# Optimization experiments

Hardware: AMD Instinct MI355X
Metric: run time of the kernel (lower is better)

## Reference

```python
import jax, jax.numpy as jnp
import numpy as np

N = 100000          # num nodes
E = 1_600_000       # num edges (avg degree 16)
IN = 512
OUT = 64
HOPS = 4


def setup_inputs() -> dict:
    key = jax.random.key(0)
    k1, k2, k3 = jax.random.split(key, 3)
    x = jax.random.normal(k1, (N, IN), dtype=jnp.float32)
    W = jax.random.normal(k2, (OUT, IN), dtype=jnp.float32) * 0.02
    b = jnp.zeros((OUT,), dtype=jnp.float32)
    edge_index = jax.random.randint(k3, (2, E), 0, N, dtype=jnp.int32)
    return {"x": x, "W": W, "b": b, "edge_index": edge_index}


def reference(x, W, b, edge_index):
    # 1) linear projection first (low-memory SGC variant)
    h = x @ W.T + b                      # [N, OUT]
    n = h.shape[0]

    # 2) gcn_norm: add self loops, symmetric D^{-1/2} A D^{-1/2}
    row, col = edge_index[0], edge_index[1]
    loop = jnp.arange(n, dtype=row.dtype)
    row = jnp.concatenate([row, loop])   # [E+N]
    col = jnp.concatenate([col, loop])
    ew = jnp.ones(row.shape[0], dtype=h.dtype)
    deg = jax.ops.segment_sum(ew, col, num_segments=n)          # in-degree incl. self loop
    dinv = jnp.where(deg > 0, jax.lax.rsqrt(deg), 0.0)
    w = dinv[row] * ew * dinv[col]       # normalized edge weights [E+N]

    # 3) hops x SpMM: adj_t built with (row=col, col=row) => out[col] += w * h[row]
    for _ in range(HOPS):
        h = jax.ops.segment_sum(w[:, None] * h[row], col, num_segments=n)
    return h
```

## Files before the change

kernel.cpp:

```cpp
#include <hip/hip_runtime.h>
#include <stdint.h>

#define IN_DIM 512
#define OUT_DIM 64

typedef short bf16x8 __attribute__((ext_vector_type(8)));
typedef float f32x4 __attribute__((ext_vector_type(4)));

__device__ inline unsigned short f2bf(float f) {
    unsigned int u = __float_as_uint(f);
    return (unsigned short)((u + 0x7FFFu + ((u >> 16) & 1u)) >> 16);
}
__device__ inline float bf2f(unsigned short s) {
    return __uint_as_float(((unsigned int)s) << 16);
}

__global__ void zero_deg_kernel(int* __restrict__ deg, int N) {
    int i = blockIdx.x * blockDim.x + threadIdx.x;
    if (i < N) deg[i] = 0;
}

__global__ void hist_kernel(const int* __restrict__ col, int* __restrict__ deg, int E) {
    int i = blockIdx.x * blockDim.x + threadIdx.x;
    if (i < E) atomicAdd(&deg[col[i]], 1);
}

__global__ void dinv_kernel(const int* __restrict__ deg, float* __restrict__ dinv,
                            float* __restrict__ d2, int N) {
    int i = blockIdx.x * blockDim.x + threadIdx.x;
    if (i < N) {
        float d = (float)deg[i] + 1.0f;
        dinv[i] = 1.0f / sqrtf(d);
        d2[i] = 1.0f / d;
    }
}

__global__ void pack_w_kernel(const float* __restrict__ W,
                              unsigned short* __restrict__ Bhi,
                              unsigned short* __restrict__ Blo) {
    int tid = blockIdx.x * blockDim.x + threadIdx.x;
    if (tid >= 4096) return;
    int L = tid & 63;
    int ct = tid >> 6;
    int t = ct & 15, c = ct >> 4;
    int o = c * 16 + (L & 15);
    int k0 = t * 32 + (L >> 4) * 8;
    const float* src = W + (size_t)o * IN_DIM + k0;
    #pragma unroll
    for (int j = 0; j < 8; ++j) {
        float w = src[j];
        unsigned short h = f2bf(w);
        Bhi[(size_t)tid * 8 + j] = h;
        Blo[(size_t)tid * 8 + j] = f2bf(w - bf2f(h));
    }
}

__global__ __launch_bounds__(1024) void scan_kernel(const int* __restrict__ deg,
                                                    int* __restrict__ rowptr,
                                                    int* __restrict__ cursor, int N) {
    __shared__ int sm[17];
    int tid = threadIdx.x, lane = tid & 63, wid = tid >> 6;
    if (tid == 0) sm[16] = 0;
    __syncthreads();
    for (int base = 0; base < N; base += 4096) {
        int i = base + tid * 4;
        int4 v = make_int4(0, 0, 0, 0);
        if (i + 3 < N) {
            v = *(const int4*)(deg + i);
        } else {
            if (i < N) v.x = deg[i];
            if (i + 1 < N) v.y = deg[i + 1];
            if (i + 2 < N) v.z = deg[i + 2];
            if (i + 3 < N) v.w = deg[i + 3];
        }
        int s1 = v.x, s2 = s1 + v.y, s3 = s2 + v.z, s4 = s3 + v.w;
        int incl = s4;
        #pragma unroll
        for (int d = 1; d < 64; d <<= 1) {
            int t = __shfl_up(incl, d, 64);
            if (lane >= d) incl += t;
        }
        __syncthreads();
        if (lane == 63) sm[wid] = incl;
        __syncthreads();
        if (tid == 0) {
            int run = sm[16];
            #pragma unroll
            for (int w2 = 0; w2 < 16; ++w2) { int t = sm[w2]; sm[w2] = run; run += t; }
            sm[16] = run;
        }
        __syncthreads();
        int tbase = incl - s4 + sm[wid];
        if (i + 3 < N) {
            int4 o = make_int4(tbase, tbase + s1, tbase + s2, tbase + s3);
            *(int4*)(rowptr + i) = o;
            *(int4*)(cursor + i) = o;
        } else {
            if (i < N)     { rowptr[i]     = tbase;      cursor[i]     = tbase; }
            if (i + 1 < N) { rowptr[i + 1] = tbase + s1; cursor[i + 1] = tbase + s1; }
            if (i + 2 < N) { rowptr[i + 2] = tbase + s2; cursor[i + 2] = tbase + s2; }
            if (i + 3 < N) { rowptr[i + 3] = tbase + s3; cursor[i + 3] = tbase + s3; }
        }
    }
    __syncthreads();
    if (tid == 0) rowptr[N] = sm[16];
}

__global__ void fill_kernel(const int* __restrict__ row, const int* __restrict__ col,
                            int* __restrict__ cursor, int* __restrict__ csr, int E) {
    int i = blockIdx.x * blockDim.x + threadIdx.x;
    if (i < E) {
        int r = row[i], c = col[i];
        int pos = atomicAdd(&cursor[c], 1);
        csr[pos] = r;
    }
}

__global__ __launch_bounds__(256) void mfma_gemm_kernel(const float* __restrict__ x,
                                                        const unsigned short* __restrict__ Bhi,
                                                        const unsigned short* __restrict__ Blo,
                                                        const float* __restrict__ bias,
                                                        const float* __restrict__ dinv,
                                                        float* __restrict__ h, int N) {
    int lane = threadIdx.x & 63;
    int wid  = __builtin_amdgcn_readfirstlane(threadIdx.x >> 6);
    int quad = lane >> 4, r16 = lane & 15;
    long rowBase = ((long)blockIdx.x * 4 + wid) * 32;
    if (rowBase >= N) return;
    bool full = (rowBase + 32 <= N);

    f32x4 acc[2][4];
    #pragma unroll
    for (int rt = 0; rt < 2; ++rt)
        #pragma unroll
        for (int c = 0; c < 4; ++c) acc[rt][c] = (f32x4){0.f, 0.f, 0.f, 0.f};

    int row0 = (int)rowBase + r16;
    int row1 = (int)rowBase + 16 + r16;
    int row0c = full ? row0 : (row0 < N ? row0 : N - 1);
    int row1c = full ? row1 : (row1 < N ? row1 : N - 1);
    const float* a0p = x + (size_t)row0c * IN_DIM + quad * 8;
    const float* a1p = x + (size_t)row1c * IN_DIM + quad * 8;

    for (int t = 0; t < 16; ++t) {
        bf16x8 bh[4], bl[4];
        #pragma unroll
        for (int c = 0; c < 4; ++c) {
            size_t off = ((size_t)(c * 16 + t) * 64 + lane) * 8;
            union { int4 i; bf16x8 b; } uh, ul;
            uh.i = *(const int4*)(Bhi + off);
            ul.i = *(const int4*)(Blo + off);
            bh[c] = uh.b; bl[c] = ul.b;
        }
        bf16x8 ah[2], al[2];
        #pragma unroll
        for (int rt = 0; rt < 2; ++rt) {
            const float* p = (rt ? a1p : a0p) + t * 32;
            float4 f0 = *(const float4*)p;
            float4 f1 = *(const float4*)(p + 4);
            float v[8] = {f0.x, f0.y, f0.z, f0.w, f1.x, f1.y, f1.z, f1.w};
            #pragma unroll
            for (int j = 0; j < 8; ++j) {
                unsigned short hi = f2bf(v[j]);
                ah[rt][j] = (short)hi;
                al[rt][j] = (short)f2bf(v[j] - bf2f(hi));
            }
        }
        #pragma unroll
        for (int rt = 0; rt < 2; ++rt)
            #pragma unroll
            for (int c = 0; c < 4; ++c) {
                acc[rt][c] = __builtin_amdgcn_mfma_f32_16x16x32_bf16(ah[rt], bh[c], acc[rt][c], 0, 0, 0);
                acc[rt][c] = __builtin_amdgcn_mfma_f32_16x16x32_bf16(ah[rt], bl[c], acc[rt][c], 0, 0, 0);
                acc[rt][c] = __builtin_amdgcn_mfma_f32_16x16x32_bf16(al[rt], bh[c], acc[rt][c], 0, 0, 0);
            }
    }

    float bb[4];
    #pragma unroll
    for (int c = 0; c < 4; ++c) bb[c] = bias[c * 16 + r16];
    #pragma unroll
    for (int rt = 0; rt < 2; ++rt)
        #pragma unroll
        for (int rr = 0; rr < 4; ++rr) {
            int row = (int)rowBase + rt * 16 + quad * 4 + rr;
            if (row < N) {
                float dv = dinv[row];
                #pragma unroll
                for (int c = 0; c < 4; ++c)
                    h[(size_t)row * OUT_DIM + c * 16 + r16] = dv * (acc[rt][c][rr] + bb[c]);
            }
        }
}

__global__ __launch_bounds__(256) void hop_kernel(const float* __restrict__ src,
                                                  float* __restrict__ dst,
                                                  const int* __restrict__ csr,
                                                  const int* __restrict__ rowptr,
                                                  const float* __restrict__ scale, int N) {
    int lane = threadIdx.x & 63;
    int wid = __builtin_amdgcn_readfirstlane(threadIdx.x >> 6);
    int node = blockIdx.x * 4 + wid;
    if (node >= N) return;
    float acc = src[(size_t)node * OUT_DIM + lane];
    int s = rowptr[node], e = rowptr[node + 1];
    int i = s;
    for (; i + 16 <= e; i += 16) {
        int idx[16];
        #pragma unroll
        for (int j = 0; j < 16; ++j) idx[j] = csr[i + j];
        float v[16];
        #pragma unroll
        for (int j = 0; j < 16; ++j) v[j] = src[(size_t)idx[j] * OUT_DIM + lane];
        float t0 = ((v[0] + v[1]) + (v[2] + v[3])) + ((v[4] + v[5]) + (v[6] + v[7]));
        float t1 = ((v[8] + v[9]) + (v[10] + v[11])) + ((v[12] + v[13]) + (v[14] + v[15]));
        acc += t0 + t1;
    }
    for (; i + 4 <= e; i += 4) {
        int i0 = csr[i], i1 = csr[i + 1], i2 = csr[i + 2], i3 = csr[i + 3];
        float v0 = src[(size_t)i0 * OUT_DIM + lane];
        float v1 = src[(size_t)i1 * OUT_DIM + lane];
        float v2 = src[(size_t)i2 * OUT_DIM + lane];
        float v3 = src[(size_t)i3 * OUT_DIM + lane];
        acc += (v0 + v1) + (v2 + v3);
    }
    for (; i < e; ++i) acc += src[(size_t)csr[i] * OUT_DIM + lane];
    dst[(size_t)node * OUT_DIM + lane] = scale[node] * acc;
}

extern "C" void kernel_launch(void* const* d_in, const int* in_sizes, int n_in,
                              void* d_out, int out_size, void* d_ws, size_t ws_size,
                              hipStream_t stream) {
    const float* x  = (const float*)d_in[0];
    const float* W  = (const float*)d_in[1];
    const float* b  = (const float*)d_in[2];
    const int*   ei = (const int*)d_in[3];
    int N = in_sizes[0] / IN_DIM;
    int E = in_sizes[3] / 2;
    const int* row = ei;
    const int* col = ei + E;
    float* out = (float*)d_out;

    float* dinv   = (float*)d_ws;
    float* d2     = dinv + N;
    int*   deg    = (int*)(d2 + N);
    int*   rowptr = deg + N;
    int*   cursor = rowptr + (N + 4);
    unsigned short* Bhi = (unsigned short*)(cursor + N);
    unsigned short* Blo = Bhi + 32768;

    float* xspace = (float*)d_in[0];
    float* hbuf   = xspace;
    int*   csr    = (int*)(xspace + (size_t)N * OUT_DIM);

    dim3 blk(256);
    int gN = (N + 255) / 256;
    int gE = (E + 255) / 256;

    zero_deg_kernel<<<gN, blk, 0, stream>>>(deg, N);
    hist_kernel<<<gE, blk, 0, stream>>>(col, deg, E);
    dinv_kernel<<<gN, blk, 0, stream>>>(deg, dinv, d2, N);

    pack_w_kernel<<<16, blk, 0, stream>>>(W, Bhi, Blo);

    mfma_gemm_kernel<<<(N + 127) / 128, blk, 0, stream>>>(x, Bhi, Blo, b, dinv, out, N);

    scan_kernel<<<1, 1024, 0, stream>>>(deg, rowptr, cursor, N);
    fill_kernel<<<gE, blk, 0, stream>>>(row, col, cursor, csr, E);

    int gH = (N + 3) / 4;
    hop_kernel<<<gH, blk, 0, stream>>>(out, hbuf, csr, rowptr, d2, N);
    hop_kernel<<<gH, blk, 0, stream>>>(hbuf, out, csr, rowptr, d2, N);
    hop_kernel<<<gH, blk, 0, stream>>>(out, hbuf, csr, rowptr, d2, N);
    hop_kernel<<<gH, blk, 0, stream>>>(hbuf, out, csr, rowptr, dinv, N);
}
```

Measured before the change: 767.7 us.

## Partition atomic histogram/fill by node range and vectorize hop gather with float4

The histogram and CSR fill kernels now use grid-stride loops in which each block handles only one of 8 node-range partitions (selected by blockIdx.x & 7). Each pass re-reads the column array but keeps its atomics within a smaller address range, with the aim of improving cache locality for the atomic counters. Separately, the hop kernel gives each quarter-wave a different edge and loads the neighbour row as float4, then combines the partial sums with cross-lane shuffles. This replaces one scalar load per lane per edge. The cost is 8 reads of the col array plus extra reductions, and the order of floating-point summation changes.

```diff
diff --git a/kernel.cpp b/kernel.cpp
--- a/kernel.cpp
+++ b/kernel.cpp
@@ -20,9 +20,17 @@
     if (i < N) deg[i] = 0;
 }
 
-__global__ void hist_kernel(const int* __restrict__ col, int* __restrict__ deg, int E) {
-    int i = blockIdx.x * blockDim.x + threadIdx.x;
-    if (i < E) atomicAdd(&deg[col[i]], 1);
+__global__ __launch_bounds__(256) void hist_part_kernel(const int* __restrict__ col,
+                                                        int* __restrict__ deg, int E, int N) {
+    int part = blockIdx.x & 7;
+    int lo = (int)((long)part * N / 8);
+    int hi = (int)((long)(part + 1) * N / 8);
+    int stride = (gridDim.x >> 3) * blockDim.x;
+    int i = (blockIdx.x >> 3) * blockDim.x + threadIdx.x;
+    for (; i < E; i += stride) {
+        int c = col[i];
+        if (c >= lo && c < hi) atomicAdd(&deg[c], 1);
+    }
 }
 
 __global__ void dinv_kernel(const int* __restrict__ deg, float* __restrict__ dinv,
@@ -106,13 +114,21 @@
     if (tid == 0) rowptr[N] = sm[16];
 }
 
-__global__ void fill_kernel(const int* __restrict__ row, const int* __restrict__ col,
-                            int* __restrict__ cursor, int* __restrict__ csr, int E) {
-    int i = blockIdx.x * blockDim.x + threadIdx.x;
-    if (i < E) {
-        int r = row[i], c = col[i];
-        int pos = atomicAdd(&cursor[c], 1);
-        csr[pos] = r;
+__global__ __launch_bounds__(256) void fill_part_kernel(const int* __restrict__ row,
+                                                        const int* __restrict__ col,
+                                                        int* __restrict__ cursor,
+                                                        int* __restrict__ csr, int E, int N) {
+    int part = blockIdx.x & 7;
+    int lo = (int)((long)part * N / 8);
+    int hi = (int)((long)(part + 1) * N / 8);
+    int stride = (gridDim.x >> 3) * blockDim.x;
+    int i = (blockIdx.x >> 3) * blockDim.x + threadIdx.x;
+    for (; i < E; i += stride) {
+        int c = col[i];
+        if (c >= lo && c < hi) {
+            int pos = atomicAdd(&cursor[c], 1);
+            csr[pos] = row[i];
+        }
     }
 }
 
@@ -200,32 +216,40 @@
                                                   const float* __restrict__ scale, int N) {
     int lane = threadIdx.x & 63;
     int wid = __builtin_amdgcn_readfirstlane(threadIdx.x >> 6);
+    int sub = lane >> 4;
+    int f4  = lane & 15;
     int node = blockIdx.x * 4 + wid;
     if (node >= N) return;
-    float acc = src[(size_t)node * OUT_DIM + lane];
+    const float4* s4 = (const float4*)src;
+
     int s = rowptr[node], e = rowptr[node + 1];
-    int i = s;
-    for (; i + 16 <= e; i += 16) {
-        int idx[16];
-        #pragma unroll
-        for (int j = 0; j < 16; ++j) idx[j] = csr[i + j];
-        float v[16];
-        #pragma unroll
-        for (int j = 0; j < 16; ++j) v[j] = src[(size_t)idx[j] * OUT_DIM + lane];
-        float t0 = ((v[0] + v[1]) + (v[2] + v[3])) + ((v[4] + v[5]) + (v[6] + v[7]));
-        float t1 = ((v[8] + v[9]) + (v[10] + v[11])) + ((v[12] + v[13]) + (v[14] + v[15]));
-        acc += t0 + t1;
-    }
-    for (; i + 4 <= e; i += 4) {
-        int i0 = csr[i], i1 = csr[i + 1], i2 = csr[i + 2], i3 = csr[i + 3];
-        float v0 = src[(size_t)i0 * OUT_DIM + lane];
-        float v1 = src[(size_t)i1 * OUT_DIM + lane];
-        float v2 = src[(size_t)i2 * OUT_DIM + lane];
-        float v3 = src[(size_t)i3 * OUT_DIM + lane];
-        acc += (v0 + v1) + (v2 + v3);
-    }
-    for (; i < e; ++i) acc += src[(size_t)csr[i] * OUT_DIM + lane];
-    dst[(size_t)node * OUT_DIM + lane] = scale[node] * acc;
+    float ax = 0.f, ay = 0.f, az = 0.f, aw = 0.f;
+    int k = s + sub;
+    for (; k + 4 < e; k += 8) {
+        int i0 = csr[k], i1 = csr[k + 4];
+        float4 v0 = s4[(size_t)i0 * 16 + f4];
+        float4 v1 = s4[(size_t)i1 * 16 + f4];
+        ax += v0.x + v1.x; ay += v0.y + v1.y;
+        az += v0.z + v1.z; aw += v0.w + v1.w;
+    }
+    if (k < e) {
+        int i0 = csr[k];
+        float4 v0 = s4[(size_t)i0 * 16 + f4];
+        ax += v0.x; ay += v0.y; az += v0.z; aw += v0.w;
+    }
+    ax += __shfl_xor(ax, 16, 64); ay += __shfl_xor(ay, 16, 64);
+    az += __shfl_xor(az, 16, 64); aw += __shfl_xor(aw, 16, 64);
+    ax += __shfl_xor(ax, 32, 64); ay += __shfl_xor(ay, 32, 64);
+    az += __shfl_xor(az, 32, 64); aw += __shfl_xor(aw, 32, 64);
+
+    if (sub == 0) {
+        float4 self = s4[(size_t)node * 16 + f4];
+        float sc = scale[node];
+        float4 o;
+        o.x = sc * (ax + self.x); o.y = sc * (ay + self.y);
+        o.z = sc * (az + self.z); o.w = sc * (aw + self.w);
+        ((float4*)dst)[(size_t)node * 16 + f4] = o;
+    }
 }
 
 extern "C" void kernel_launch(void* const* d_in, const int* in_sizes, int n_in,
@@ -255,10 +279,10 @@
 
     dim3 blk(256);
     int gN = (N + 255) / 256;
-    int gE = (E + 255) / 256;
+    int gPart = 8 * 784;
 
     zero_deg_kernel<<<gN, blk, 0, stream>>>(deg, N);
-    hist_kernel<<<gE, blk, 0, stream>>>(col, deg, E);
+    hist_part_kernel<<<gPart, blk, 0, stream>>>(col, deg, E, N);
     dinv_kernel<<<gN, blk, 0, stream>>>(deg, dinv, d2, N);
 
     pack_w_kernel<<<16, blk, 0, stream>>>(W, Bhi, Blo);
@@ -266,7 +290,7 @@
     mfma_gemm_kernel<<<(N + 127) / 128, blk, 0, stream>>>(x, Bhi, Blo, b, dinv, out, N);
 
     scan_kernel<<<1, 1024, 0, stream>>>(deg, rowptr, cursor, N);
-    fill_kernel<<<gE, blk, 0, stream>>>(row, col, cursor, csr, E);
+    fill_part_kernel<<<gPart, blk, 0, stream>>>(row, col, cursor, csr, E, N);
 
     int gH = (N + 3) / 4;
     hop_kernel<<<gH, blk, 0, stream>>>(out, hbuf, csr, rowptr, d2, N);
```

Result: faster. 736.6 us (-4.1%).
